# Kernel optimization log

Measured on AMD Instinct MI355X. Metric: run time of the kernel, lower is better.

Reference implementation:

```python
import jax, jax.numpy as jnp
import numpy as np

B, M, Q, D = 32, 8192, 64, 128

def setup_inputs() -> dict:
    key = jax.random.key(0)
    k1, k2, k3, k4 = jax.random.split(key, 4)
    story_a = jax.random.normal(k1, (B, M, D), dtype=jnp.float32)
    u = jax.random.normal(k2, (B, Q, D), dtype=jnp.float32)
    story_c = jax.random.normal(k3, (B, M, D), dtype=jnp.float32)
    H = jax.random.normal(k4, (D, D), dtype=jnp.float32) * (1.0 / np.sqrt(D))
    return {"story_a": story_a, "u": u, "story_c": story_c, "H": H}

def reference(story_a, u, story_c, H):
    # scores: Dot(axes=-1)([story_a, u]) -> (B, M, Q)
    m = jnp.einsum('bmd,bqd->bmq', story_a, u)
    # Keras Softmax() default axis=-1: normalize over Q (faithful to original)
    p = jax.nn.softmax(m, axis=-1)          # (B, M, Q)
    p = jnp.swapaxes(p, 1, 2)                # (B, Q, M)
    # output memory: Dot(axes=(2,1))([p, story_c]) -> (B, Q, D)
    c = jnp.einsum('bqm,bmd->bqd', p, story_c)
    # linear residual: K.dot(u, H) + c
    mapped_u = jnp.einsum('bqd,de->bqe', u, H)
    return c + mapped_u
```

## Files before the change

kernel.cpp:

```cpp
#include <hip/hip_runtime.h>

#define B_ 32
#define M_ 8192
#define Q_ 64
#define D_ 128
#define MT 64
#define LDA 136
#define LDP 72

typedef __attribute__((ext_vector_type(8))) short short8;
typedef __attribute__((ext_vector_type(4))) float floatx4;

__device__ __forceinline__ unsigned short f2bf(float x) {
  union { float f; unsigned u; } t; t.f = x;
  unsigned r = t.u + 0x7fffu + ((t.u >> 16) & 1u);
  return (unsigned short)(r >> 16);
}

__global__ __launch_bounds__(256, 2) void memn2n_main(
    const float* __restrict__ A, const float* __restrict__ U,
    const float* __restrict__ Cc, float* __restrict__ dst,
    int chunks, int use_atomic) {
  __shared__ __align__(16) unsigned short sU[Q_ * LDA];
  __shared__ __align__(16) unsigned short sA[MT * LDA];
  __shared__ __align__(16) unsigned short sC[MT * LDA];
  __shared__ __align__(16) unsigned short sP[Q_ * LDP];

  const int tid  = threadIdx.x;
  const int lane = tid & 63;
  const int w    = tid >> 6;
  const int l15  = lane & 15;
  const int quad = (lane >> 4) & 3;

  const int blk = blockIdx.x;
  const int b   = blk / chunks;
  const int ch  = blk - b * chunks;
  const int Mc  = M_ / chunks;
  const int m0  = ch * Mc;

  const int g = tid & 31;
  const int r = tid >> 5;

  const float* ub = U + (size_t)b * Q_ * D_;
#pragma unroll
  for (int i = 0; i < 8; ++i) {
    int row = r + 8 * i;
    float4 v = *(const float4*)(ub + row * D_ + 4 * g);
    ushort4 h = make_ushort4(f2bf(v.x), f2bf(v.y), f2bf(v.z), f2bf(v.w));
    *(ushort4*)&sU[row * LDA + 4 * g] = h;
  }

  floatx4 acc[2][4];
#pragma unroll
  for (int i = 0; i < 2; ++i)
#pragma unroll
    for (int j = 0; j < 4; ++j) acc[i][j] = (floatx4){0.f, 0.f, 0.f, 0.f};

  const float* Abase = A + (size_t)b * M_ * D_ + (size_t)m0 * D_;
  const float* Cbase = Cc + (size_t)b * M_ * D_ + (size_t)m0 * D_;

  const int nT = Mc / MT;
  for (int t = 0; t < nT; ++t) {
    __syncthreads();
    const float* At = Abase + (size_t)t * MT * D_;
    const float* Ct = Cbase + (size_t)t * MT * D_;
#pragma unroll
    for (int i = 0; i < 8; ++i) {
      int mi = r + 8 * i;
      float4 va = *(const float4*)(At + mi * D_ + 4 * g);
      float4 vc = *(const float4*)(Ct + mi * D_ + 4 * g);
      ushort4 ha = make_ushort4(f2bf(va.x), f2bf(va.y), f2bf(va.z), f2bf(va.w));
      ushort4 hc = make_ushort4(f2bf(vc.x), f2bf(vc.y), f2bf(vc.z), f2bf(vc.w));
      *(ushort4*)&sA[mi * LDA + 4 * g] = ha;
      *(ushort4*)&sC[mi * LDA + 4 * g] = hc;
    }
    __syncthreads();

    floatx4 s1[4];
#pragma unroll
    for (int qs = 0; qs < 4; ++qs) s1[qs] = (floatx4){0.f, 0.f, 0.f, 0.f};
#pragma unroll
    for (int ks = 0; ks < 4; ++ks) {
      short8 af = *(const short8*)&sA[(16 * w + l15) * LDA + 32 * ks + 8 * quad];
#pragma unroll
      for (int qs = 0; qs < 4; ++qs) {
        short8 bfv = *(const short8*)&sU[(16 * qs + l15) * LDA + 32 * ks + 8 * quad];
        s1[qs] = __builtin_amdgcn_mfma_f32_16x16x32_bf16(af, bfv, s1[qs], 0, 0, 0);
      }
    }

    float pv[4][4];
#pragma unroll
    for (int rg = 0; rg < 4; ++rg) {
      float v0 = s1[0][rg], v1 = s1[1][rg], v2 = s1[2][rg], v3 = s1[3][rg];
      float mx = fmaxf(fmaxf(v0, v1), fmaxf(v2, v3));
#pragma unroll
      for (int m = 1; m <= 8; m <<= 1) mx = fmaxf(mx, __shfl_xor(mx, m, 64));
      const float c = 1.4426950408889634f;
      float e0 = exp2f((v0 - mx) * c), e1 = exp2f((v1 - mx) * c);
      float e2 = exp2f((v2 - mx) * c), e3 = exp2f((v3 - mx) * c);
      float sm = e0 + e1 + e2 + e3;
#pragma unroll
      for (int m = 1; m <= 8; m <<= 1) sm += __shfl_xor(sm, m, 64);
      float inv = 1.0f / sm;
      pv[0][rg] = e0 * inv; pv[1][rg] = e1 * inv;
      pv[2][rg] = e2 * inv; pv[3][rg] = e3 * inv;
    }
#pragma unroll
    for (int qs = 0; qs < 4; ++qs) {
      ushort4 h = make_ushort4(f2bf(pv[qs][0]), f2bf(pv[qs][1]),
                               f2bf(pv[qs][2]), f2bf(pv[qs][3]));
      *(ushort4*)&sP[(16 * qs + l15) * LDP + 16 * w + 4 * quad] = h;
    }
    __syncthreads();

#pragma unroll
    for (int ks = 0; ks < 2; ++ks) {
      short8 pa[4];
#pragma unroll
      for (int qs = 0; qs < 4; ++qs)
        pa[qs] = *(const short8*)&sP[(16 * qs + l15) * LDP + 32 * ks + 8 * quad];
#pragma unroll
      for (int ds = 0; ds < 2; ++ds) {
        int d = l15 + 16 * (2 * w + ds);
        union { unsigned short u[8]; short8 v; } bb;
#pragma unroll
        for (int j = 0; j < 8; ++j)
          bb.u[j] = sC[(32 * ks + 8 * quad + j) * LDA + d];
#pragma unroll
        for (int qs = 0; qs < 4; ++qs)
          acc[ds][qs] = __builtin_amdgcn_mfma_f32_16x16x32_bf16(pa[qs], bb.v, acc[ds][qs], 0, 0, 0);
      }
    }
  }

  if (use_atomic) {
#pragma unroll
    for (int ds = 0; ds < 2; ++ds)
#pragma unroll
      for (int qs = 0; qs < 4; ++qs)
#pragma unroll
        for (int rg = 0; rg < 4; ++rg) {
          int q = qs * 16 + quad * 4 + rg;
          int d = l15 + 16 * (2 * w + ds);
          atomicAdd(&dst[((size_t)b * Q_ + q) * D_ + d], acc[ds][qs][rg]);
        }
  } else {
    float* pp = dst + (((size_t)ch * B_ + b) * Q_) * D_;
#pragma unroll
    for (int ds = 0; ds < 2; ++ds)
#pragma unroll
      for (int qs = 0; qs < 4; ++qs)
#pragma unroll
        for (int rg = 0; rg < 4; ++rg) {
          int q = qs * 16 + quad * 4 + rg;
          int d = l15 + 16 * (2 * w + ds);
          pp[q * D_ + d] = acc[ds][qs][rg];
        }
  }
}

__global__ __launch_bounds__(128) void memn2n_reduce(
    const float* __restrict__ U, const float* __restrict__ H,
    const float* __restrict__ part, float* __restrict__ out, int chunks) {
  int bq = blockIdx.x;
  int b = bq >> 6, q = bq & 63;
  int d = threadIdx.x;
  __shared__ float su[D_];
  size_t row = ((size_t)b * Q_ + q) * D_;
  su[d] = U[row + d];
  __syncthreads();
  float acc = 0.f;
#pragma unroll 16
  for (int e = 0; e < D_; ++e) acc = fmaf(su[e], H[e * D_ + d], acc);
  for (int ch = 0; ch < chunks; ++ch)
    acc += part[(((size_t)ch * B_ + b) * Q_ + q) * D_ + d];
  out[row + d] = acc;
}

extern "C" void kernel_launch(void* const* d_in, const int* in_sizes, int n_in,
                              void* d_out, int out_size, void* d_ws, size_t ws_size,
                              hipStream_t stream) {
  const float* A  = (const float*)d_in[0];
  const float* U  = (const float*)d_in[1];
  const float* Cc = (const float*)d_in[2];
  const float* H  = (const float*)d_in[3];
  float* out = (float*)d_out;

  const int CH = 16;
  size_t need = (size_t)CH * B_ * Q_ * D_ * sizeof(float);
  if (ws_size >= need) {
    float* part = (float*)d_ws;
    memn2n_main<<<B_ * CH, 256, 0, stream>>>(A, U, Cc, part, CH, 0);
    memn2n_reduce<<<B_ * Q_, 128, 0, stream>>>(U, H, part, out, CH);
  } else {
    memn2n_reduce<<<B_ * Q_, 128, 0, stream>>>(U, H, nullptr, out, 0);
    memn2n_main<<<B_ * 8, 256, 0, stream>>>(A, U, Cc, out, 8, 1);
  }
}
```

Measured before the change: 300.9 us.

## Prepack U fragments, alias LDS buffers, drop softmax max, raise occupancy and chunks

```diff
diff --git a/kernel.cpp b/kernel.cpp
--- a/kernel.cpp
+++ b/kernel.cpp
@@ -11,20 +11,49 @@
 typedef __attribute__((ext_vector_type(8))) short short8;
 typedef __attribute__((ext_vector_type(4))) float floatx4;
 
-__device__ __forceinline__ unsigned short f2bf(float x) {
-  union { float f; unsigned u; } t; t.f = x;
-  unsigned r = t.u + 0x7fffu + ((t.u >> 16) & 1u);
-  return (unsigned short)(r >> 16);
-}
-
-__global__ __launch_bounds__(256, 2) void memn2n_main(
-    const float* __restrict__ A, const float* __restrict__ U,
-    const float* __restrict__ Cc, float* __restrict__ dst,
+__device__ __forceinline__ unsigned pkbf(float a, float b) {
+  unsigned ua = __builtin_bit_cast(unsigned, a) + 0x8000u;
+  unsigned ub = __builtin_bit_cast(unsigned, b) + 0x8000u;
+  return __builtin_amdgcn_perm(ub, ua, 0x07060302u);
+}
+
+template <int CTRL>
+__device__ __forceinline__ float dppadd(float x) {
+  int y = __builtin_amdgcn_update_dpp(0, __builtin_bit_cast(int, x), CTRL, 0xF, 0xF, true);
+  return x + __builtin_bit_cast(float, y);
+}
+__device__ __forceinline__ float rowsum16(float x) {
+  x = dppadd<0x128>(x); x = dppadd<0x124>(x);
+  x = dppadd<0x122>(x); x = dppadd<0x121>(x);
+  return x;
+}
+
+__device__ __forceinline__ void barrier_lds() {
+  asm volatile("s_waitcnt lgkmcnt(0)\n\ts_barrier" ::: "memory");
+}
+
+__global__ __launch_bounds__(256) void pack_u(const float* __restrict__ U,
+                                              short8* __restrict__ ufrag) {
+  int t = blockIdx.x * 256 + threadIdx.x;
+  int lane = t & 63, ks = (t >> 6) & 3, qs = (t >> 8) & 3, b = t >> 10;
+  int l15 = lane & 15, quad = (lane >> 4) & 3;
+  const float* p = U + ((size_t)b * Q_ + 16 * qs + l15) * D_ + 32 * ks + 8 * quad;
+  float4 x = *(const float4*)p;
+  float4 y = *(const float4*)(p + 4);
+  union { unsigned u[4]; short8 v; } o;
+  o.u[0] = pkbf(x.x, x.y); o.u[1] = pkbf(x.z, x.w);
+  o.u[2] = pkbf(y.x, y.y); o.u[3] = pkbf(y.z, y.w);
+  ufrag[t] = o.v;
+}
+
+__global__ __launch_bounds__(256, 4) void memn2n_main(
+    const float* __restrict__ A, const float* __restrict__ Cc,
+    const short8* __restrict__ ufrag, float* __restrict__ dst,
     int chunks, int use_atomic) {
-  __shared__ __align__(16) unsigned short sU[Q_ * LDA];
-  __shared__ __align__(16) unsigned short sA[MT * LDA];
+  __shared__ __align__(16) unsigned short sAP[MT * LDA];
   __shared__ __align__(16) unsigned short sC[MT * LDA];
-  __shared__ __align__(16) unsigned short sP[Q_ * LDP];
+  unsigned short* const sA = sAP;
+  unsigned short* const sP = sAP;
 
   const int tid  = threadIdx.x;
   const int lane = tid & 63;
@@ -36,19 +65,12 @@
   const int b   = blk / chunks;
   const int ch  = blk - b * chunks;
   const int Mc  = M_ / chunks;
-  const int m0  = ch * Mc;
+  const int nT  = Mc / MT;
 
   const int g = tid & 31;
   const int r = tid >> 5;
 
-  const float* ub = U + (size_t)b * Q_ * D_;
-#pragma unroll
-  for (int i = 0; i < 8; ++i) {
-    int row = r + 8 * i;
-    float4 v = *(const float4*)(ub + row * D_ + 4 * g);
-    ushort4 h = make_ushort4(f2bf(v.x), f2bf(v.y), f2bf(v.z), f2bf(v.w));
-    *(ushort4*)&sU[row * LDA + 4 * g] = h;
-  }
+  const short8* ufb = ufrag + (size_t)b * 16 * 64 + lane;
 
   floatx4 acc[2][4];
 #pragma unroll
@@ -56,25 +78,26 @@
 #pragma unroll
     for (int j = 0; j < 4; ++j) acc[i][j] = (floatx4){0.f, 0.f, 0.f, 0.f};
 
-  const float* Abase = A + (size_t)b * M_ * D_ + (size_t)m0 * D_;
-  const float* Cbase = Cc + (size_t)b * M_ * D_ + (size_t)m0 * D_;
-
-  const int nT = Mc / MT;
+  const float* Abase = A + ((size_t)b * M_ + (size_t)ch * Mc) * D_;
+  const float* Cbase = Cc + ((size_t)b * M_ + (size_t)ch * Mc) * D_;
+
   for (int t = 0; t < nT; ++t) {
-    __syncthreads();
     const float* At = Abase + (size_t)t * MT * D_;
     const float* Ct = Cbase + (size_t)t * MT * D_;
+    barrier_lds();
 #pragma unroll
     for (int i = 0; i < 8; ++i) {
       int mi = r + 8 * i;
-      float4 va = *(const float4*)(At + mi * D_ + 4 * g);
-      float4 vc = *(const float4*)(Ct + mi * D_ + 4 * g);
-      ushort4 ha = make_ushort4(f2bf(va.x), f2bf(va.y), f2bf(va.z), f2bf(va.w));
-      ushort4 hc = make_ushort4(f2bf(vc.x), f2bf(vc.y), f2bf(vc.z), f2bf(vc.w));
-      *(ushort4*)&sA[mi * LDA + 4 * g] = ha;
-      *(ushort4*)&sC[mi * LDA + 4 * g] = hc;
-    }
-    __syncthreads();
+      float4 v = *(const float4*)(At + mi * D_ + 4 * g);
+      *(uint2*)&sA[mi * LDA + 4 * g] = make_uint2(pkbf(v.x, v.y), pkbf(v.z, v.w));
+    }
+#pragma unroll
+    for (int i = 0; i < 8; ++i) {
+      int mi = r + 8 * i;
+      float4 v = *(const float4*)(Ct + mi * D_ + 4 * g);
+      *(uint2*)&sC[mi * LDA + 4 * g] = make_uint2(pkbf(v.x, v.y), pkbf(v.z, v.w));
+    }
+    barrier_lds();
 
     floatx4 s1[4];
 #pragma unroll
@@ -84,35 +107,30 @@
       short8 af = *(const short8*)&sA[(16 * w + l15) * LDA + 32 * ks + 8 * quad];
 #pragma unroll
       for (int qs = 0; qs < 4; ++qs) {
-        short8 bfv = *(const short8*)&sU[(16 * qs + l15) * LDA + 32 * ks + 8 * quad];
+        short8 bfv = ufb[(qs * 4 + ks) * 64];
         s1[qs] = __builtin_amdgcn_mfma_f32_16x16x32_bf16(af, bfv, s1[qs], 0, 0, 0);
       }
     }
+    barrier_lds();
 
     float pv[4][4];
 #pragma unroll
     for (int rg = 0; rg < 4; ++rg) {
-      float v0 = s1[0][rg], v1 = s1[1][rg], v2 = s1[2][rg], v3 = s1[3][rg];
-      float mx = fmaxf(fmaxf(v0, v1), fmaxf(v2, v3));
-#pragma unroll
-      for (int m = 1; m <= 8; m <<= 1) mx = fmaxf(mx, __shfl_xor(mx, m, 64));
       const float c = 1.4426950408889634f;
-      float e0 = exp2f((v0 - mx) * c), e1 = exp2f((v1 - mx) * c);
-      float e2 = exp2f((v2 - mx) * c), e3 = exp2f((v3 - mx) * c);
-      float sm = e0 + e1 + e2 + e3;
-#pragma unroll
-      for (int m = 1; m <= 8; m <<= 1) sm += __shfl_xor(sm, m, 64);
-      float inv = 1.0f / sm;
+      float e0 = exp2f(s1[0][rg] * c), e1 = exp2f(s1[1][rg] * c);
+      float e2 = exp2f(s1[2][rg] * c), e3 = exp2f(s1[3][rg] * c);
+      float sm = (e0 + e1) + (e2 + e3);
+      sm = rowsum16(sm);
+      float inv = __builtin_amdgcn_rcpf(sm);
       pv[0][rg] = e0 * inv; pv[1][rg] = e1 * inv;
       pv[2][rg] = e2 * inv; pv[3][rg] = e3 * inv;
     }
 #pragma unroll
     for (int qs = 0; qs < 4; ++qs) {
-      ushort4 h = make_ushort4(f2bf(pv[qs][0]), f2bf(pv[qs][1]),
-                               f2bf(pv[qs][2]), f2bf(pv[qs][3]));
-      *(ushort4*)&sP[(16 * qs + l15) * LDP + 16 * w + 4 * quad] = h;
-    }
-    __syncthreads();
+      *(uint2*)&sP[(16 * qs + l15) * LDP + 16 * w + 4 * quad] =
+          make_uint2(pkbf(pv[qs][0], pv[qs][1]), pkbf(pv[qs][2], pv[qs][3]));
+    }
+    barrier_lds();
 
 #pragma unroll
     for (int ks = 0; ks < 2; ++ks) {
@@ -173,6 +191,7 @@
   float acc = 0.f;
 #pragma unroll 16
   for (int e = 0; e < D_; ++e) acc = fmaf(su[e], H[e * D_ + d], acc);
+#pragma unroll 8
   for (int ch = 0; ch < chunks; ++ch)
     acc += part[(((size_t)ch * B_ + b) * Q_ + q) * D_ + d];
   out[row + d] = acc;
@@ -187,14 +206,32 @@
   const float* H  = (const float*)d_in[3];
   float* out = (float*)d_out;
 
-  const int CH = 16;
-  size_t need = (size_t)CH * B_ * Q_ * D_ * sizeof(float);
-  if (ws_size >= need) {
+  const size_t upack_bytes = (size_t)B_ * 16 * 64 * 16;
+
+  int CHn = 32;
+  size_t part_bytes = (size_t)CHn * B_ * Q_ * D_ * sizeof(float);
+  if (ws_size >= part_bytes + upack_bytes) {
     float* part = (float*)d_ws;
-    memn2n_main<<<B_ * CH, 256, 0, stream>>>(A, U, Cc, part, CH, 0);
-    memn2n_reduce<<<B_ * Q_, 128, 0, stream>>>(U, H, part, out, CH);
-  } else {
+    short8* upk = (short8*)((char*)d_ws + part_bytes);
+    pack_u<<<128, 256, 0, stream>>>(U, upk);
+    memn2n_main<<<B_ * CHn, 256, 0, stream>>>(A, Cc, upk, part, CHn, 0);
+    memn2n_reduce<<<B_ * Q_, 128, 0, stream>>>(U, H, part, out, CHn);
+    return;
+  }
+  CHn = 16;
+  part_bytes = (size_t)CHn * B_ * Q_ * D_ * sizeof(float);
+  if (ws_size >= part_bytes + upack_bytes) {
+    float* part = (float*)d_ws;
+    short8* upk = (short8*)((char*)d_ws + part_bytes);
+    pack_u<<<128, 256, 0, stream>>>(U, upk);
+    memn2n_main<<<B_ * CHn, 256, 0, stream>>>(A, Cc, upk, part, CHn, 0);
+    memn2n_reduce<<<B_ * Q_, 128, 0, stream>>>(U, H, part, out, CHn);
+    return;
+  }
+  {
+    short8* upk = (short8*)d_ws;
+    pack_u<<<128, 256, 0, stream>>>(U, upk);
     memn2n_reduce<<<B_ * Q_, 128, 0, stream>>>(U, H, nullptr, out, 0);
-    memn2n_main<<<B_ * 8, 256, 0, stream>>>(A, U, Cc, out, 8, 1);
-  }
-}
+    memn2n_main<<<B_ * 8, 256, 0, stream>>>(A, Cc, upk, out, 8, 1);
+  }
+}
```

Result: slower. 309.4 us (+2.8%).
